# Performance work log

Measured on AMD Instinct MI355X. Metric: run time of the kernel, lower is better.

The kernel has to match this reference:

```python
import math
import jax, jax.numpy as jnp
import numpy as np

H = 8
C_HIDDEN = 32
C_Q = 256


def setup_inputs() -> dict:
    key = jax.random.key(0)
    ks = jax.random.split(key, 9)
    B, S, Q, K = 1, 128, 256, 256
    q_x = jax.random.normal(ks[0], (B, S, Q, C_Q), dtype=jnp.float32)
    kv_x = jax.random.normal(ks[1], (B, S, K, C_Q), dtype=jnp.float32)
    bias1 = jax.random.normal(ks[2], (B, S, 1, 1, K), dtype=jnp.float32)
    bias2 = jax.random.normal(ks[3], (B, 1, H, Q, K), dtype=jnp.float32)
    scale = 1.0 / math.sqrt(C_Q)
    wq = jax.random.normal(ks[4], (H * C_HIDDEN, C_Q), dtype=jnp.float32) * scale
    wk = jax.random.normal(ks[5], (H * C_HIDDEN, C_Q), dtype=jnp.float32) * scale
    wv = jax.random.normal(ks[6], (H * C_HIDDEN, C_Q), dtype=jnp.float32) * scale
    wg = jax.random.normal(ks[7], (H * C_HIDDEN, C_Q), dtype=jnp.float32) * scale
    wo = jax.random.normal(ks[8], (C_Q, H * C_HIDDEN), dtype=jnp.float32) * scale
    return {"q_x": q_x, "kv_x": kv_x, "bias1": bias1, "bias2": bias2,
            "wq": wq, "wk": wk, "wv": wv, "wg": wg, "wo": wo}


def _split_heads(x):
    # [..., L, H*c] -> [..., H, L, c]
    y = x.reshape(x.shape[:-1] + (H, C_HIDDEN))
    return jnp.moveaxis(y, -2, -3)


def reference(q_x, kv_x, bias1, bias2, wq, wk, wv, wg, wo):
    # QKV projections (no bias), per-head split, scale q by 1/sqrt(c_hidden)
    q = _split_heads(q_x @ wq.T) / math.sqrt(C_HIDDEN)   # [B,S,H,Q,c]
    k = _split_heads(kv_x @ wk.T)                         # [B,S,H,K,c]
    v = _split_heads(kv_x @ wv.T)                         # [B,S,H,K,c]
    # attention logits with additive biases folded in
    a = jnp.einsum('...hqc,...hkc->...hqk', q, k) + bias1 + bias2
    a = jax.nn.softmax(a, axis=-1)
    o = jnp.einsum('...hqk,...hkc->...hqc', a, v)         # [B,S,H,Q,c]
    o = jnp.moveaxis(o, -3, -2)                           # [B,S,Q,H,c]
    # sigmoid gating from query data
    g = jax.nn.sigmoid(q_x @ wg.T)                        # [B,S,Q,H*c]
    g = g.reshape(g.shape[:-1] + (H, C_HIDDEN))
    o = o * g
    o = o.reshape(o.shape[:-2] + (H * C_HIDDEN,))         # flatten heads
    return o @ wo.T                                       # [B,S,Q,C_Q]
```

## Files before the change

### kernel.cpp

```cpp
#include <hip/hip_runtime.h>
#include <math.h>

#define S_DIM 128
#define H_DIM 8
#define M_TOT (S_DIM * 256)

typedef unsigned short ushort_t;
typedef unsigned int   uint32;
typedef __bf16  v8bf  __attribute__((ext_vector_type(8)));
typedef float   v4f   __attribute__((ext_vector_type(4)));
typedef uint32  u32x4 __attribute__((ext_vector_type(4)));

__device__ inline ushort_t f2b(float x) {
    unsigned int u = __float_as_uint(x);
    u += 0x7fffu + ((u >> 16) & 1u);
    return (ushort_t)(u >> 16);
}
__device__ inline float b2f(ushort_t h) {
    return __uint_as_float(((unsigned int)h) << 16);
}

__device__ inline uint32 pack2(float e0, float e1) {
    return __builtin_amdgcn_perm(__float_as_uint(e1) + 0x8000u,
                                 __float_as_uint(e0) + 0x8000u, 0x07060302u);
}
__device__ inline void split_pair(float e0, float e1, uint32& hp, uint32& lp) {
    hp = pack2(e0, e1);
    const float h0 = __uint_as_float(hp << 16);
    const float h1 = __uint_as_float(hp & 0xffff0000u);
    lp = pack2(e0 - h0, e1 - h1);
}
__device__ inline void cvt_split8(v4f a, v4f b, v8bf& h, v8bf& l) {
    uint32 h0, h1, h2, h3, l0, l1, l2, l3;
    split_pair(a[0], a[1], h0, l0); split_pair(a[2], a[3], h1, l1);
    split_pair(b[0], b[1], h2, l2); split_pair(b[2], b[3], h3, l3);
    u32x4 hp = {h0, h1, h2, h3}, lp = {l0, l1, l2, l3};
    h = *(v8bf*)&hp; l = *(v8bf*)&lp;
}

#define GLDS16(gp, lp) __builtin_amdgcn_global_load_lds( \
    (const __attribute__((address_space(1))) void*)(gp), \
    (__attribute__((address_space(3))) void*)(lp), 16, 0, 0)

__global__ __launch_bounds__(256) void split_w(
    const float* __restrict__ w0, const float* __restrict__ w1,
    const float* __restrict__ w2, const float* __restrict__ w3,
    const float* __restrict__ w4,
    ushort_t* __restrict__ hi, ushort_t* __restrict__ lo)
{
    const float* src;
    switch (blockIdx.y) {
        case 0: src = w0; break; case 1: src = w1; break;
        case 2: src = w2; break; case 3: src = w3; break;
        default: src = w4; break;
    }
    int i = blockIdx.x * 256 + threadIdx.x;
    float4 v = ((const float4*)src)[i];
    ushort4 h, l;
    h.x = f2b(v.x); l.x = f2b(v.x - b2f(h.x));
    h.y = f2b(v.y); l.y = f2b(v.y - b2f(h.y));
    h.z = f2b(v.z); l.z = f2b(v.z - b2f(h.z));
    h.w = f2b(v.w); l.w = f2b(v.w - b2f(h.w));
    size_t base = (size_t)blockIdx.y * 16384;
    ((ushort4*)hi)[base + i] = h;
    ((ushort4*)lo)[base + i] = l;
}


__global__ __launch_bounds__(256) void gemm_proj(
    const float* __restrict__ xq, const float* __restrict__ xkv,
    const ushort_t* __restrict__ Whi4, const ushort_t* __restrict__ Wlo4,
    ushort_t* __restrict__ qh, ushort_t* __restrict__ ql,
    ushort_t* __restrict__ kh, ushort_t* __restrict__ kl,
    float* __restrict__ g_out,
    ushort_t* __restrict__ vh,
    float qscale)
{
    __shared__ float    ldsA[2][4096];
    __shared__ ushort_t ldsW[2][2][4096];

    const int z    = blockIdx.z;
    const int L    = blockIdx.x + 4 * blockIdx.y;
    const int mti  = ((L >> 5) << 3) + (L & 7);
    const int nti  = (L >> 3) & 3;
    const int t    = threadIdx.x;
    const int l    = t & 63;
    const int wv   = t >> 6;
    const int wm   = wv & 1;
    const int wn   = wv >> 1;
    const int idx  = l & 15;
    const int quad = l >> 4;
    const int m0   = mti * 128;
    const int n0   = nti * 128;

    const float* Asrc = (z ? xkv : xq) + (size_t)m0 * 256;
    const ushort_t* Whi = Whi4 + (size_t)z * 131072 + (size_t)n0 * 256;
    const ushort_t* Wlo = Wlo4 + (size_t)z * 131072 + (size_t)n0 * 256;
    const float scale = z ? 1.f : qscale;

    size_t stA[4];
    #pragma unroll
    for (int j = 0; j < 4; ++j) {
        const int slot = j * 256 + t;
        const int c2 = slot >> 9, row = (slot >> 2) & 127, seg = slot & 3;
        const int gseg = (seg - (row >> 1)) & 3;
        stA[j] = (size_t)row * 256 + c2 * 16 + gseg * 4;
    }
    size_t stW[2]; int sdW[2];
    #pragma unroll
    for (int i = 0; i < 2; ++i) {
        const int sb   = wv * 128 + i * 64;
        const int slot = sb + l;
        const int row  = slot >> 2;
        const int gseg = ((slot & 3) - (row >> 1)) & 3;
        stW[i] = (size_t)row * 256 + gseg * 8;
        sdW[i] = sb * 8;
    }

    v4f acc[4][4];
    #pragma unroll
    for (int i = 0; i < 4; ++i)
        #pragma unroll
        for (int j = 0; j < 4; ++j) acc[i][j] = (v4f){0.f, 0.f, 0.f, 0.f};

    #pragma unroll
    for (int j = 0; j < 4; ++j)
        GLDS16(Asrc + stA[j], &ldsA[0][(j * 256 + wv * 64) * 4]);
    #pragma unroll
    for (int i = 0; i < 2; ++i) {
        GLDS16(Whi + stW[i], &ldsW[0][0][sdW[i]]);
        GLDS16(Wlo + stW[i], &ldsW[0][1][sdW[i]]);
    }
    __builtin_amdgcn_s_waitcnt(0);
    __syncthreads();

    const int c2 = quad >> 1;
    const int s0 = (quad & 1) * 2;

    int cur = 0;
    for (int k0 = 0; k0 < 256; k0 += 32) {
        if (k0 < 224) {
            #pragma unroll
            for (int j = 0; j < 4; ++j)
                GLDS16(Asrc + stA[j] + k0 + 32, &ldsA[cur ^ 1][(j * 256 + wv * 64) * 4]);
            #pragma unroll
            for (int i = 0; i < 2; ++i) {
                GLDS16(Whi + stW[i] + k0 + 32, &ldsW[cur ^ 1][0][sdW[i]]);
                GLDS16(Wlo + stW[i] + k0 + 32, &ldsW[cur ^ 1][1][sdW[i]]);
            }
        }

        v8bf ah[4], al[4], bh[4], bl[4];
        #pragma unroll
        for (int mt = 0; mt < 4; ++mt) {
            const int r  = wm * 64 + mt * 16 + idx;
            const int rb = c2 * 2048 + r * 16;
            v4f fa = *(const v4f*)&ldsA[cur][rb + (((s0 + (r >> 1)) & 3) << 2)];
            v4f fb = *(const v4f*)&ldsA[cur][rb + (((s0 + 1 + (r >> 1)) & 3) << 2)];
            cvt_split8(fa, fb, ah[mt], al[mt]);
        }
        #pragma unroll
        for (int nt = 0; nt < 4; ++nt) {
            const int r   = wn * 64 + nt * 16 + idx;
            const int off = r * 32 + (((quad + (r >> 1)) & 3) << 3);
            bh[nt] = *(const v8bf*)&ldsW[cur][0][off];
            bl[nt] = *(const v8bf*)&ldsW[cur][1][off];
        }

        #pragma unroll
        for (int mt = 0; mt < 4; ++mt)
            #pragma unroll
            for (int nt = 0; nt < 4; ++nt) {
                acc[mt][nt] = __builtin_amdgcn_mfma_f32_16x16x32_bf16(ah[mt], bh[nt], acc[mt][nt], 0, 0, 0);
                acc[mt][nt] = __builtin_amdgcn_mfma_f32_16x16x32_bf16(al[mt], bh[nt], acc[mt][nt], 0, 0, 0);
                acc[mt][nt] = __builtin_amdgcn_mfma_f32_16x16x32_bf16(ah[mt], bl[nt], acc[mt][nt], 0, 0, 0);
            }

        __builtin_amdgcn_s_waitcnt(0);
        __syncthreads();
        cur ^= 1;
    }

    ushort_t* dsth = z ? kh : qh;
    ushort_t* dstl = z ? kl : ql;

    #pragma unroll
    for (int mt = 0; mt < 4; ++mt) {
        const int mbase = m0 + wm * 64 + mt * 16 + quad * 4;
        const int s = mbase >> 8, r8 = mbase & 255;
        #pragma unroll
        for (int nt = 0; nt < 4; ++nt) {
            const int gcol = n0 + wn * 64 + nt * 16 + idx;
            if (gcol < 256) {
                const int hh = gcol >> 5, c = gcol & 31;
                const size_t di = (((size_t)(s * 8 + hh) * 256) + r8) * 32 + c;
                #pragma unroll
                for (int r = 0; r < 4; ++r) {
                    const float val = acc[mt][nt][r] * scale;
                    const ushort_t hv = f2b(val);
                    dsth[di + (size_t)r * 32] = hv;
                    dstl[di + (size_t)r * 32] = f2b(val - b2f(hv));
                }
            } else if (z == 0) {
                const int gc = gcol - 256;
                #pragma unroll
                for (int r = 0; r < 4; ++r)
                    g_out[(size_t)(mbase + r) * 256 + gc] = acc[mt][nt][r];
            } else {
                const int gc = gcol - 256, hh = gc >> 5, c = gc & 31;
                ushort4 hv4;
                #pragma unroll
                for (int r = 0; r < 4; ++r)
                    ((ushort_t*)&hv4)[r] = f2b(acc[mt][nt][r]);
                const size_t di = (((size_t)(s * 8 + hh) * 32) + c) * 256 + r8;
                *(ushort4*)&vh[di] = hv4;
            }
        }
    }
}

__global__ __launch_bounds__(256) void gemm_out(
    const ushort_t* __restrict__ Ah, const ushort_t* __restrict__ Whi,
    const ushort_t* __restrict__ Wlo, float* __restrict__ Cf)
{
    __shared__ ushort_t lds[2][3][128 * 32];

    const int L    = blockIdx.x + 2 * blockIdx.y;
    const int mti  = ((L >> 4) << 3) + (L & 7);
    const int nti  = (L >> 3) & 1;
    const int t    = threadIdx.x;
    const int l    = t & 63;
    const int wv   = t >> 6;
    const int wm   = wv & 1;
    const int wn   = wv >> 1;
    const int idx  = l & 15;
    const int quad = l >> 4;
    const int m0   = mti * 128;
    const int n0   = nti * 128;

    const ushort_t* srcs[3] = { Ah + (size_t)m0 * 256,
                                Whi + (size_t)n0 * 256, Wlo + (size_t)n0 * 256 };

    size_t stoff[2]; int sdst[2];
    #pragma unroll
    for (int i = 0; i < 2; ++i) {
        const int sb   = wv * 128 + i * 64;
        const int slot = sb + l;
        const int row  = slot >> 2;
        const int gseg = ((slot & 3) - (row >> 1)) & 3;
        stoff[i] = (size_t)row * 256 + gseg * 8;
        sdst[i]  = sb * 8;
    }

    v4f acc[4][4];
    #pragma unroll
    for (int i = 0; i < 4; ++i)
        #pragma unroll
        for (int j = 0; j < 4; ++j) acc[i][j] = (v4f){0.f, 0.f, 0.f, 0.f};

    #pragma unroll
    for (int b = 0; b < 3; ++b)
        #pragma unroll
        for (int i = 0; i < 2; ++i)
            GLDS16(srcs[b] + stoff[i], &lds[0][b][sdst[i]]);
    __builtin_amdgcn_s_waitcnt(0);
    __syncthreads();

    int cur = 0;
    for (int k0 = 0; k0 < 256; k0 += 32) {
        if (k0 < 224) {
            #pragma unroll
            for (int b = 0; b < 3; ++b)
                #pragma unroll
                for (int i = 0; i < 2; ++i)
                    GLDS16(srcs[b] + stoff[i] + k0 + 32, &lds[cur ^ 1][b][sdst[i]]);
        }

        v8bf ah[4], bh[4], bl[4];
        #pragma unroll
        for (int mt = 0; mt < 4; ++mt) {
            const int r   = wm * 64 + mt * 16 + idx;
            const int off = r * 32 + (((quad + (r >> 1)) & 3) << 3);
            ah[mt] = *(const v8bf*)&lds[cur][0][off];
        }
        #pragma unroll
        for (int nt = 0; nt < 4; ++nt) {
            const int r   = wn * 64 + nt * 16 + idx;
            const int off = r * 32 + (((quad + (r >> 1)) & 3) << 3);
            bh[nt] = *(const v8bf*)&lds[cur][1][off];
            bl[nt] = *(const v8bf*)&lds[cur][2][off];
        }

        #pragma unroll
        for (int mt = 0; mt < 4; ++mt)
            #pragma unroll
            for (int nt = 0; nt < 4; ++nt) {
                acc[mt][nt] = __builtin_amdgcn_mfma_f32_16x16x32_bf16(ah[mt], bh[nt], acc[mt][nt], 0, 0, 0);
                acc[mt][nt] = __builtin_amdgcn_mfma_f32_16x16x32_bf16(ah[mt], bl[nt], acc[mt][nt], 0, 0, 0);
            }

        __builtin_amdgcn_s_waitcnt(0);
        __syncthreads();
        cur ^= 1;
    }

    #pragma unroll
    for (int mt = 0; mt < 4; ++mt) {
        #pragma unroll
        for (int nt = 0; nt < 4; ++nt) {
            const int gcol = n0 + wn * 64 + nt * 16 + idx;
            #pragma unroll
            for (int r = 0; r < 4; ++r) {
                const int grow = m0 + wm * 64 + mt * 16 + quad * 4 + r;
                Cf[(size_t)grow * 256 + gcol] = acc[mt][nt][r];
            }
        }
    }
}

__global__ __launch_bounds__(256, 2) void attn_mfma(
    const ushort_t* __restrict__ qh, const ushort_t* __restrict__ ql,
    const ushort_t* __restrict__ kh, const ushort_t* __restrict__ kl,
    const ushort_t* __restrict__ vth,
    const float* __restrict__ b1, const float* __restrict__ b2,
    const float* __restrict__ gbuf,
    ushort_t* __restrict__ oh)
{
    __shared__ __align__(16) uint32   pbuf[4][64 * 36];
    __shared__ __align__(16) ushort_t kst[2][3][2048];
    __shared__ __align__(16) float    invl[4][64];

    const int sh = blockIdx.x, s = sh >> 3, h = sh & 7;
    const int t = threadIdx.x, l = t & 63, w = t >> 6;
    const int idx = l & 15, quad = l >> 4;

    const size_t shb = (size_t)sh * 8192;
    const ushort_t* qhp = qh + shb;
    const ushort_t* qlp = ql + shb;
    const ushort_t* khp = kh + shb;
    const ushort_t* klp = kl + shb;
    const ushort_t* vhp = vth + shb;
    const float* b1p = b1 + (size_t)s * 256;
    const float* b2p = b2 + (size_t)h * 65536;

    const int ksrow = t >> 2;
    const int ksseg = ((t & 3) - (ksrow >> 1)) & 3;
    const size_t koff = (size_t)ksrow * 32 + ksseg * 8;
    const int vc   = (t >> 2) & 31;
    const int vkt  = t >> 7;
    const int vseg = ((t & 3) - (vc >> 1)) & 3;
    const size_t voff = (size_t)vc * 256 + vkt * 32 + vseg * 8;
    const int wbase = w * 512;

    v8bf qfh[4], qfl[4];
    #pragma unroll
    for (int nt = 0; nt < 4; ++nt) {
        const int off = (w * 64 + nt * 16 + idx) * 32 + quad * 8;
        qfh[nt] = *(const v8bf*)(qhp + off);
        qfl[nt] = *(const v8bf*)(qlp + off);
    }

    v4f oacc[4][2];
    #pragma unroll
    for (int mt = 0; mt < 4; ++mt) {
        oacc[mt][0] = (v4f){0.f, 0.f, 0.f, 0.f};
        oacc[mt][1] = (v4f){0.f, 0.f, 0.f, 0.f};
    }
    float lrun[4] = {0.f, 0.f, 0.f, 0.f};

    GLDS16(khp + koff, &kst[0][0][wbase]);
    GLDS16(klp + koff, &kst[0][1][wbase]);
    GLDS16(vhp + voff, &kst[0][2][wbase]);
    __builtin_amdgcn_s_waitcnt(0);
    __syncthreads();

    for (int c4 = 0; c4 < 4; ++c4) {
        const int ak0 = c4 * 64;
        const int cur = c4 & 1;

        if (c4 < 3) {
            const size_t nb = (size_t)(ak0 + 64) * 32;
            GLDS16(khp + nb + koff, &kst[cur ^ 1][0][wbase]);
            GLDS16(klp + nb + koff, &kst[cur ^ 1][1][wbase]);
            GLDS16(vhp + (ak0 + 64) + voff, &kst[cur ^ 1][2][wbase]);
        }

        v8bf kfh[4], kfl[4];
        #pragma unroll
        for (int at = 0; at < 4; ++at) {
            const int row = at * 16 + idx;
            const int off = row * 32 + (((quad + (row >> 1)) & 3) << 3);
            kfh[at] = *(const v8bf*)&kst[cur][0][off];
            kfl[at] = *(const v8bf*)&kst[cur][1][off];
        }

        v4f sacc[4][4];
        #pragma unroll
        for (int at = 0; at < 4; ++at)
            #pragma unroll
            for (int nt = 0; nt < 4; ++nt)
                sacc[at][nt] = (v4f){0.f, 0.f, 0.f, 0.f};
        __builtin_amdgcn_s_setprio(1);
        #pragma unroll
        for (int at = 0; at < 4; ++at)
            #pragma unroll
            for (int nt = 0; nt < 4; ++nt) {
                sacc[at][nt] = __builtin_amdgcn_mfma_f32_16x16x32_bf16(kfh[at], qfh[nt], sacc[at][nt], 0, 0, 0);
                sacc[at][nt] = __builtin_amdgcn_mfma_f32_16x16x32_bf16(kfl[at], qfh[nt], sacc[at][nt], 0, 0, 0);
                sacc[at][nt] = __builtin_amdgcn_mfma_f32_16x16x32_bf16(kfh[at], qfl[nt], sacc[at][nt], 0, 0, 0);
            }
        __builtin_amdgcn_s_setprio(0);

        v8bf vfh[2][2];
        #pragma unroll
        for (int n2 = 0; n2 < 2; ++n2)
            #pragma unroll
            for (int kt = 0; kt < 2; ++kt) {
                const int c  = n2 * 16 + idx;
                const int sp = (quad + (c >> 1)) & 3;
                vfh[n2][kt] = *(const v8bf*)&kst[cur][2][kt * 1024 + c * 32 + sp * 8];
            }

        v4f b1v[4];
        #pragma unroll
        for (int at = 0; at < 4; ++at)
            b1v[at] = *(const v4f*)(b1p + ak0 + at * 16 + quad * 4);

        #pragma unroll
        for (int at = 0; at < 4; ++at)
            #pragma unroll
            for (int nt = 0; nt < 4; ++nt) {
                const int q = w * 64 + nt * 16 + idx;
                v4f b2v = *(const v4f*)(b2p + (size_t)q * 256 + ak0 + at * 16 + quad * 4);
                float e0 = __expf(b1v[at][0] + b2v[0] + sacc[at][nt][0]);
                float e1 = __expf(b1v[at][1] + b2v[1] + sacc[at][nt][1]);
                float e2 = __expf(b1v[at][2] + b2v[2] + sacc[at][nt][2]);
                float e3 = __expf(b1v[at][3] + b2v[3] + sacc[at][nt][3]);
                lrun[nt] += (e0 + e1) + (e2 + e3);
                uint32 p0 = pack2(e0, e1);
                uint32 p1 = pack2(e2, e3);
                const int dw = (nt * 16 + idx) * 36 + at * 8 + quad * 2;
                *(uint2*)&pbuf[w][dw] = make_uint2(p0, p1);
            }

        __builtin_amdgcn_s_setprio(1);
        #pragma unroll
        for (int mt = 0; mt < 4; ++mt)
            #pragma unroll
            for (int kt = 0; kt < 2; ++kt) {
                v8bf pf = *(const v8bf*)&pbuf[w][(mt * 16 + idx) * 36 + kt * 16 + quad * 4];
                #pragma unroll
                for (int n2 = 0; n2 < 2; ++n2)
                    oacc[mt][n2] = __builtin_amdgcn_mfma_f32_16x16x32_bf16(pf, vfh[n2][kt], oacc[mt][n2], 0, 0, 0);
            }
        __builtin_amdgcn_s_setprio(0);

        __builtin_amdgcn_s_waitcnt(0);
        __syncthreads();
    }

    #pragma unroll
    for (int nt = 0; nt < 4; ++nt) {
        float v = lrun[nt];
        v += __shfl_xor(v, 16, 64);
        v += __shfl_xor(v, 32, 64);
        if (quad == 0) invl[w][nt * 16 + idx] = 1.f / v;
    }

    #pragma unroll
    for (int mt = 0; mt < 4; ++mt) {
        v4f iv = *(const v4f*)&invl[w][mt * 16 + quad * 4];
        #pragma unroll
        for (int n2 = 0; n2 < 2; ++n2) {
            const int c = n2 * 16 + idx;
            #pragma unroll
            for (int r = 0; r < 4; ++r) {
                const int q = w * 64 + mt * 16 + quad * 4 + r;
                const size_t gi = (size_t)(s * 256 + q) * 256 + h * 32 + c;
                const float gv = gbuf[gi];
                const float sig = 1.f / (1.f + __expf(-gv));
                oh[gi] = f2b(oacc[mt][n2][r] * iv[r] * sig);
            }
        }
    }
}

extern "C" void kernel_launch(void* const* d_in, const int* in_sizes, int n_in,
                              void* d_out, int out_size, void* d_ws, size_t ws_size,
                              hipStream_t stream)
{
    const float* q_x   = (const float*)d_in[0];
    const float* kv_x  = (const float*)d_in[1];
    const float* bias1 = (const float*)d_in[2];
    const float* bias2 = (const float*)d_in[3];
    const float* wq    = (const float*)d_in[4];
    const float* wk    = (const float*)d_in[5];
    const float* wv    = (const float*)d_in[6];
    const float* wg    = (const float*)d_in[7];
    const float* wo    = (const float*)d_in[8];
    float* out = (float*)d_out;

    const size_t BUF = (size_t)M_TOT * 256;

    float*    g_buf = (float*)d_ws;
    ushort_t* p     = (ushort_t*)(g_buf + BUF);
    ushort_t* qhb = p;            ushort_t* qlb = qhb + BUF;
    ushort_t* khb = qlb + BUF;    ushort_t* klb = khb + BUF;
    ushort_t* vhb = klb + BUF;
    ushort_t* ohb = vhb + BUF;
    ushort_t* w_hi = ohb + BUF;
    ushort_t* w_lo = w_hi + 5 * 65536;

    const float qscale = 0.17677669529663689f;

    split_w<<<dim3(64, 5), 256, 0, stream>>>(wq, wg, wk, wv, wo, w_hi, w_lo);

    gemm_proj<<<dim3(4, 256, 2), 256, 0, stream>>>(
        q_x, kv_x, w_hi, w_lo, qhb, qlb, khb, klb, g_buf, vhb, qscale);

    attn_mfma<<<S_DIM * H_DIM, 256, 0, stream>>>(
        qhb, qlb, khb, klb, vhb, bias1, bias2, g_buf, ohb);

    gemm_out<<<dim3(2, 256), 256, 0, stream>>>(
        ohb, w_hi + 4 * 65536, w_lo + 4 * 65536, out);
}
```

Measured before the change: 267.7 us.

## Split A tile to bf16 hi/lo once at staging instead of per-wave in LDS reads

The projection GEMM now loads fp32 activation chunks into registers, splits them into bf16 hi/lo pairs, and writes the packed halves into LDS, replacing async global-to-LDS copies of fp32 plus per-fragment conversion. Previously each wave converted its A fragments on every k-step, so the same rows were split redundantly by the two column waves. Doing the split once at staging, after the MFMAs, is meant to cut conversion ALU work and halve LDS read bytes for A. In exchange the A prefetch now goes through registers, which raises register pressure and makes the MFMA phase wait on global loads rather than the async LDS path.

```diff
diff --git a/kernel.cpp b/kernel.cpp
--- a/kernel.cpp
+++ b/kernel.cpp
@@ -9,7 +9,6 @@
 typedef unsigned int   uint32;
 typedef __bf16  v8bf  __attribute__((ext_vector_type(8)));
 typedef float   v4f   __attribute__((ext_vector_type(4)));
-typedef uint32  u32x4 __attribute__((ext_vector_type(4)));
 
 __device__ inline ushort_t f2b(float x) {
     unsigned int u = __float_as_uint(x);
@@ -30,12 +29,9 @@
     const float h1 = __uint_as_float(hp & 0xffff0000u);
     lp = pack2(e0 - h0, e1 - h1);
 }
-__device__ inline void cvt_split8(v4f a, v4f b, v8bf& h, v8bf& l) {
-    uint32 h0, h1, h2, h3, l0, l1, l2, l3;
-    split_pair(a[0], a[1], h0, l0); split_pair(a[2], a[3], h1, l1);
-    split_pair(b[0], b[1], h2, l2); split_pair(b[2], b[3], h3, l3);
-    u32x4 hp = {h0, h1, h2, h3}, lp = {l0, l1, l2, l3};
-    h = *(v8bf*)&hp; l = *(v8bf*)&lp;
+__device__ inline void split4(v4f a, uint32& h0, uint32& h1, uint32& l0, uint32& l1) {
+    split_pair(a[0], a[1], h0, l0);
+    split_pair(a[2], a[3], h1, l1);
 }
 
 #define GLDS16(gp, lp) __builtin_amdgcn_global_load_lds( \
@@ -76,7 +72,7 @@
     ushort_t* __restrict__ vh,
     float qscale)
 {
-    __shared__ float    ldsA[2][4096];
+    __shared__ ushort_t ldsA[2][2][4096];
     __shared__ ushort_t ldsW[2][2][4096];
 
     const int z    = blockIdx.z;
@@ -98,13 +94,14 @@
     const ushort_t* Wlo = Wlo4 + (size_t)z * 131072 + (size_t)n0 * 256;
     const float scale = z ? 1.f : qscale;
 
-    size_t stA[4];
+    size_t agoff[4]; int adoff[4];
     #pragma unroll
     for (int j = 0; j < 4; ++j) {
         const int slot = j * 256 + t;
-        const int c2 = slot >> 9, row = (slot >> 2) & 127, seg = slot & 3;
-        const int gseg = (seg - (row >> 1)) & 3;
-        stA[j] = (size_t)row * 256 + c2 * 16 + gseg * 4;
+        const int row = slot >> 3, c8 = slot & 7;
+        agoff[j] = (size_t)row * 256 + c8 * 4;
+        const int segp = ((c8 >> 1) + (row >> 1)) & 3;
+        adoff[j] = row * 32 + segp * 8 + (c8 & 1) * 4;
     }
     size_t stW[2]; int sdW[2];
     #pragma unroll
@@ -123,26 +120,34 @@
         #pragma unroll
         for (int j = 0; j < 4; ++j) acc[i][j] = (v4f){0.f, 0.f, 0.f, 0.f};
 
-    #pragma unroll
-    for (int j = 0; j < 4; ++j)
-        GLDS16(Asrc + stA[j], &ldsA[0][(j * 256 + wv * 64) * 4]);
-    #pragma unroll
-    for (int i = 0; i < 2; ++i) {
-        GLDS16(Whi + stW[i], &ldsW[0][0][sdW[i]]);
-        GLDS16(Wlo + stW[i], &ldsW[0][1][sdW[i]]);
-    }
-    __builtin_amdgcn_s_waitcnt(0);
-    __syncthreads();
-
-    const int c2 = quad >> 1;
-    const int s0 = (quad & 1) * 2;
+    {
+        v4f areg[4];
+        #pragma unroll
+        for (int j = 0; j < 4; ++j)
+            areg[j] = *(const v4f*)(Asrc + agoff[j]);
+        #pragma unroll
+        for (int i = 0; i < 2; ++i) {
+            GLDS16(Whi + stW[i], &ldsW[0][0][sdW[i]]);
+            GLDS16(Wlo + stW[i], &ldsW[0][1][sdW[i]]);
+        }
+        #pragma unroll
+        for (int j = 0; j < 4; ++j) {
+            uint32 h0, h1, l0, l1;
+            split4(areg[j], h0, h1, l0, l1);
+            *(uint2*)&ldsA[0][0][adoff[j]] = make_uint2(h0, h1);
+            *(uint2*)&ldsA[0][1][adoff[j]] = make_uint2(l0, l1);
+        }
+        __builtin_amdgcn_s_waitcnt(0);
+        __syncthreads();
+    }
 
     int cur = 0;
     for (int k0 = 0; k0 < 256; k0 += 32) {
+        v4f anext[4];
         if (k0 < 224) {
             #pragma unroll
             for (int j = 0; j < 4; ++j)
-                GLDS16(Asrc + stA[j] + k0 + 32, &ldsA[cur ^ 1][(j * 256 + wv * 64) * 4]);
+                anext[j] = *(const v4f*)(Asrc + agoff[j] + k0 + 32);
             #pragma unroll
             for (int i = 0; i < 2; ++i) {
                 GLDS16(Whi + stW[i] + k0 + 32, &ldsW[cur ^ 1][0][sdW[i]]);
@@ -153,11 +158,10 @@
         v8bf ah[4], al[4], bh[4], bl[4];
         #pragma unroll
         for (int mt = 0; mt < 4; ++mt) {
-            const int r  = wm * 64 + mt * 16 + idx;
-            const int rb = c2 * 2048 + r * 16;
-            v4f fa = *(const v4f*)&ldsA[cur][rb + (((s0 + (r >> 1)) & 3) << 2)];
-            v4f fb = *(const v4f*)&ldsA[cur][rb + (((s0 + 1 + (r >> 1)) & 3) << 2)];
-            cvt_split8(fa, fb, ah[mt], al[mt]);
+            const int r   = wm * 64 + mt * 16 + idx;
+            const int off = r * 32 + (((quad + (r >> 1)) & 3) << 3);
+            ah[mt] = *(const v8bf*)&ldsA[cur][0][off];
+            al[mt] = *(const v8bf*)&ldsA[cur][1][off];
         }
         #pragma unroll
         for (int nt = 0; nt < 4; ++nt) {
@@ -175,6 +179,16 @@
                 acc[mt][nt] = __builtin_amdgcn_mfma_f32_16x16x32_bf16(al[mt], bh[nt], acc[mt][nt], 0, 0, 0);
                 acc[mt][nt] = __builtin_amdgcn_mfma_f32_16x16x32_bf16(ah[mt], bl[nt], acc[mt][nt], 0, 0, 0);
             }
+
+        if (k0 < 224) {
+            #pragma unroll
+            for (int j = 0; j < 4; ++j) {
+                uint32 h0, h1, l0, l1;
+                split4(anext[j], h0, h1, l0, l1);
+                *(uint2*)&ldsA[cur ^ 1][0][adoff[j]] = make_uint2(h0, h1);
+                *(uint2*)&ldsA[cur ^ 1][1][adoff[j]] = make_uint2(l0, l1);
+            }
+        }
 
         __builtin_amdgcn_s_waitcnt(0);
         __syncthreads();
```

Result: no change. 265.2 us (-0.9%).
